# Performance work log

Hardware: AMD Instinct MI355X
Metric: run time of the kernel (lower is better)

The kernel has to match this reference:

```python
import jax, jax.numpy as jnp
import numpy as np

B, S, V, E, H, L = 64, 512, 32000, 512, 512, 2


def setup_inputs() -> dict:
    key = jax.random.key(0)
    ks = jax.random.split(key, 8)
    x = jax.random.randint(ks[0], (B, S), 0, V, dtype=jnp.int64 if jax.config.jax_enable_x64 else jnp.int32)
    # pack_right_padded_seq assumes right-padded seqs; hidden[:ebs] slicing implies
    # lengths sorted in DESCENDING order. Enforce length >= 1.
    lengths = jnp.clip(jax.random.randint(ks[1], (B,), 0, S + 1), 1, S)
    lengths = jnp.sort(lengths)[::-1]
    scale = 1.0 / np.sqrt(H)
    emb = jax.random.normal(ks[2], (V, E), dtype=jnp.float32) * 0.02
    W_ih = jax.random.uniform(ks[3], (L, H, E), jnp.float32, -scale, scale)
    W_hh = jax.random.uniform(ks[4], (L, H, H), jnp.float32, -scale, scale)
    b_ih = jax.random.uniform(ks[5], (L, H), jnp.float32, -scale, scale)
    b_hh = jax.random.uniform(ks[6], (L, H), jnp.float32, -scale, scale)
    return {"x": x, "lengths": lengths, "emb": emb, "W_ih": W_ih,
            "W_hh": W_hh, "b_ih": b_ih, "b_hh": b_hh}


def reference(x, lengths, emb, W_ih, W_hh, b_ih, b_hh):
    # Equivalent to the packed-sequence loop: at timestep t, only sequences with
    # t < length are active (packing with descending lengths keeps them as the
    # leading rows). We express the same math with a mask + lax.scan.
    xe = jnp.swapaxes(emb[x], 0, 1)                       # [S, B, E]
    mask = jnp.arange(S)[:, None] < lengths[None, :]      # [S, B]
    h0 = jnp.zeros((B, L, H), dtype=emb.dtype)

    def step(h, inp):
        xt, m = inp                                        # [B,E], [B]
        cur = xt
        hs = []
        for l in range(L):
            hl = h[:, l]                                   # [B, H]
            hn = jnp.tanh(cur @ W_ih[l].T + b_ih[l] + hl @ W_hh[l].T + b_hh[l])
            hl = jnp.where(m[:, None], hn, hl)             # freeze finished seqs
            hs.append(hl)
            cur = hl                                       # next layer's input
        return jnp.stack(hs, axis=1), None

    hidden, _ = jax.lax.scan(step, h0, (xe, mask))
    out = hidden[:, -1]                                    # last layer final state
    return out, hidden
```

## Files before the change

kernel.cpp:

```cpp
#include <hip/hip_runtime.h>


#define BATCH 64
#define SEQ   512
#define HID   512
#define NTHR  256
#define CB    8
#define ROWS  32
#define SLOT  (BATCH * HID)

typedef unsigned int u32;
typedef unsigned long long u64;
#define POISON 0xFFFFFFFFFFFFFFFFull

__device__ __forceinline__ float dot4(const float4 a, const float4 b) {
  return a.x * b.x + a.y * b.y + a.z * b.z + a.w * b.w;
}
__device__ __forceinline__ float2 ld2(const double* p) {
  const double d = __hip_atomic_load(p, __ATOMIC_RELAXED, __HIP_MEMORY_SCOPE_AGENT);
  return __builtin_bit_cast(float2, d);
}
__device__ __forceinline__ u64 ldu(const double* p) {
  const double d = __hip_atomic_load(p, __ATOMIC_RELAXED, __HIP_MEMORY_SCOPE_AGENT);
  return __builtin_bit_cast(u64, d);
}
__device__ __forceinline__ void st2(double* p, float2 v) {
  __hip_atomic_store(p, __builtin_bit_cast(double, v),
                     __ATOMIC_RELAXED, __HIP_MEMORY_SCOPE_AGENT);
}
__device__ __forceinline__ float tanh_fast(float x) {
  const float a = fabsf(x);
  const float e = __expf(-2.0f * a);
  const float t = (1.0f - e) * __builtin_amdgcn_rcpf(1.0f + e);
  return copysignf(t, x);
}
#define WAIT_VM0() asm volatile("s_waitcnt vmcnt(0)" ::: "memory")

#define RSTEP(D, N)                                                   \
  {                                                                   \
    const bool hi = (lane & (D)) != 0;                                \
    _Pragma("unroll")                                                 \
    for (int a = 0; a < (N); ++a) {                                   \
      const float keep = hi ? v[a + (N)] : v[a];                      \
      const float send = hi ? v[a] : v[a + (N)];                      \
      v[a] = keep + __shfl_xor(send, (D));                            \
    }                                                                 \
  }

template <bool NP>
__global__ __launch_bounds__(NTHR, 1) void rnn_persistent(
    const int* __restrict__ x, const int* __restrict__ lengths,
    const float* __restrict__ emb,
    const float* __restrict__ W_ih, const float* __restrict__ W_hh,
    const float* __restrict__ b_ih, const float* __restrict__ b_hh,
    float* __restrict__ out,
    float* h0r, float* h1r, u32* F, int ring)
{
  __shared__ __align__(16) float Xa[CB][HID];
  __shared__ __align__(16) float Xb[CB][HID];
  __shared__ __align__(16) float Xpart[CB][ROWS][4];
  __shared__ int Lens[CB];

  const int wg    = blockIdx.x;
  const int tid   = threadIdx.x;
  const int dom   = wg & 7;
  const int q     = wg >> 3;
  const int layer = q >> 4;
  const int rg    = q & 15;
  const int bbase = dom * CB;
  const int jbase = rg * ROWS;
  const int tj    = tid >> 6;
  const int lane  = tid & 63;

  u32* Fown = F + ((dom * 2 + layer) * 16 + rg) * 32;
  u32* F0   = F + ((dom * 2 + 0) * 16) * 32;
  u32* F1   = F + ((dom * 2 + 1) * 16) * 32;

  float4 wa[2][8], wb[2][8];
  {
    const float* WA = W_ih + layer * (HID * HID);
    const float* WB = W_hh + layer * (HID * HID);
    #pragma unroll
    for (int ji = 0; ji < 8; ++ji) {
      const int j = jbase + tj * 8 + ji;
      #pragma unroll
      for (int i = 0; i < 2; ++i) {
        const int k = i * 256 + 4 * lane;
        wa[i][ji] = *(const float4*)&WA[j * HID + k];
        wb[i][ji] = *(const float4*)&WB[j * HID + k];
      }
    }
  }
  if (tid < CB) Lens[tid] = lengths[bbase + tid];
  __syncthreads();
  int maxlen = Lens[0];
  #pragma unroll
  for (int i = 1; i < CB; ++i) maxlen = max(maxlen, Lens[i]);
  const int P     = maxlen;
  const int pl0   = (P < SEQ) ? P : (SEQ - 1);
  const int plast = layer ? P : pl0;
  int lm[4];
  #pragma unroll
  for (int g = 0; g < 4; ++g) lm[g] = max(Lens[2 * g], Lens[2 * g + 1]);

  float4 bias4 = make_float4(0.f, 0.f, 0.f, 0.f);
  if (tid < 64) {
    const int jq = jbase + (tid & 7) * 4;
    bias4.x = b_ih[layer * HID + jq + 0] + b_hh[layer * HID + jq + 0];
    bias4.y = b_ih[layer * HID + jq + 1] + b_hh[layer * HID + jq + 1];
    bias4.z = b_ih[layer * HID + jq + 2] + b_hh[layer * HID + jq + 2];
    bias4.w = b_ih[layer * HID + jq + 3] + b_hh[layer * HID + jq + 3];
  }

  float4 pf[4];
  if (layer == 0) {
    #pragma unroll
    for (int i = 0; i < 4; ++i) {
      const int u = tid + NTHR * i;
      const int r = u >> 7, c = (u & 127) * 4;
      const int tok = x[(bbase + r) * SEQ];
      pf[i] = *(const float4*)&emb[(size_t)tok * HID + c];
    }
  }

  int cur = 0, prev = ring - 1;

  for (int p = 0; p <= P; ++p) {
    const bool active = layer ? (p >= 1) : (p < SEQ);
    const int  wr0    = (cur + 1 == ring) ? 0 : (cur + 1);

    if (active) {
      const int t = layer ? (p - 1) : p;

      if (layer == 0) {
        const double* src = (const double*)(h0r) + (size_t)cur * (SLOT / 2);
        if constexpr (NP) {
          u64 tv[8];
          #pragma unroll
          for (int i = 0; i < 8; ++i) {
            const int u = tid + NTHR * i;
            tv[i] = ldu(&src[(size_t)(bbase + (u >> 8)) * 256 + (u & 255)]);
          }
          for (;;) {
            u32 bad = 0;
            #pragma unroll
            for (int i = 0; i < 8; ++i) bad |= (tv[i] == POISON) ? (1u << i) : 0u;
            if (!bad) break;
            #pragma unroll
            for (int i = 0; i < 8; ++i)
              if (bad & (1u << i)) {
                const int u = tid + NTHR * i;
                tv[i] = ldu(&src[(size_t)(bbase + (u >> 8)) * 256 + (u & 255)]);
              }
          }
          #pragma unroll
          for (int i = 0; i < 8; ++i) {
            const int u = tid + NTHR * i;
            *(float2*)&Xb[u >> 8][(u & 255) * 2] = __builtin_bit_cast(float2, tv[i]);
          }
        } else {
          float2 tv[8];
          #pragma unroll
          for (int i = 0; i < 8; ++i) {
            const int u = tid + NTHR * i;
            tv[i] = ld2(&src[(size_t)(bbase + (u >> 8)) * 256 + (u & 255)]);
          }
          #pragma unroll
          for (int i = 0; i < 8; ++i) {
            const int u = tid + NTHR * i;
            *(float2*)&Xb[u >> 8][(u & 255) * 2] = tv[i];
          }
        }
        #pragma unroll
        for (int i = 0; i < 4; ++i) {
          const int u = tid + NTHR * i;
          *(float4*)&Xa[u >> 7][(u & 127) * 4] = pf[i];
        }
      } else {
        const double* srcB = (const double*)(h1r) + (size_t)prev * (SLOT / 2);
        const double* srcA = (const double*)(h0r) + (size_t)cur  * (SLOT / 2);
        if constexpr (NP) {
          u64 tb[8], ta[8];
          #pragma unroll
          for (int i = 0; i < 8; ++i) {
            const int u = tid + NTHR * i;
            tb[i] = ldu(&srcB[(size_t)(bbase + (u >> 8)) * 256 + (u & 255)]);
          }
          #pragma unroll
          for (int i = 0; i < 8; ++i) {
            const int u = tid + NTHR * i;
            ta[i] = ldu(&srcA[(size_t)(bbase + (u >> 8)) * 256 + (u & 255)]);
          }
          for (;;) {
            u32 bad = 0;
            #pragma unroll
            for (int i = 0; i < 8; ++i) {
              bad |= (tb[i] == POISON) ? (1u << i) : 0u;
              bad |= (ta[i] == POISON) ? (1u << (i + 8)) : 0u;
            }
            if (!bad) break;
            #pragma unroll
            for (int i = 0; i < 8; ++i) {
              const int u = tid + NTHR * i;
              if (bad & (1u << i))
                tb[i] = ldu(&srcB[(size_t)(bbase + (u >> 8)) * 256 + (u & 255)]);
              if (bad & (1u << (i + 8)))
                ta[i] = ldu(&srcA[(size_t)(bbase + (u >> 8)) * 256 + (u & 255)]);
            }
          }
          #pragma unroll
          for (int i = 0; i < 8; ++i) {
            const int u = tid + NTHR * i;
            *(float2*)&Xb[u >> 8][(u & 255) * 2] = __builtin_bit_cast(float2, tb[i]);
            *(float2*)&Xa[u >> 8][(u & 255) * 2] = __builtin_bit_cast(float2, ta[i]);
          }
        } else {
          float2 tb[8], ta[8];
          #pragma unroll
          for (int i = 0; i < 8; ++i) {
            const int u = tid + NTHR * i;
            tb[i] = ld2(&srcB[(size_t)(bbase + (u >> 8)) * 256 + (u & 255)]);
          }
          #pragma unroll
          for (int i = 0; i < 8; ++i) {
            const int u = tid + NTHR * i;
            ta[i] = ld2(&srcA[(size_t)(bbase + (u >> 8)) * 256 + (u & 255)]);
          }
          #pragma unroll
          for (int i = 0; i < 8; ++i) {
            const int u = tid + NTHR * i;
            *(float2*)&Xb[u >> 8][(u & 255) * 2] = tb[i];
            *(float2*)&Xa[u >> 8][(u & 255) * 2] = ta[i];
          }
        }
      }
      __syncthreads();

      #pragma unroll 2
      for (int g = 0; g < 4; ++g) {
        if (t >= lm[g]) continue;
        float v[16];
        #pragma unroll
        for (int o = 0; o < 16; ++o) v[o] = 0.f;
        #pragma unroll
        for (int bi = 0; bi < 2; ++bi) {
          const int b = g * 2 + bi;
          const float4 xa0 = *(const float4*)&Xa[b][4 * lane];
          const float4 xa1 = *(const float4*)&Xa[b][256 + 4 * lane];
          const float4 xb0 = *(const float4*)&Xb[b][4 * lane];
          const float4 xb1 = *(const float4*)&Xb[b][256 + 4 * lane];
          #pragma unroll
          for (int ji = 0; ji < 8; ++ji) {
            v[bi * 8 + ji] += dot4(wa[0][ji], xa0) + dot4(wa[1][ji], xa1)
                            + dot4(wb[0][ji], xb0) + dot4(wb[1][ji], xb1);
          }
        }
        RSTEP(32, 8)
        RSTEP(16, 4)
        RSTEP(8, 2)
        RSTEP(4, 1)
        const int b_o = g * 2 + (lane >> 5);
        const int j_o = tj * 8 + ((lane >> 2) & 7);
        Xpart[b_o][j_o][lane & 3] = v[0];
      }
      __syncthreads();

      if (tid < 64) {
        const int b = tid >> 3, jq = (tid & 7) * 4;
        const float4 hb = *(const float4*)&Xb[b][jbase + jq];
        const bool live = (t < Lens[b]);
        float4 r = hb;
        if (live) {
          const float4 p0 = *(const float4*)&Xpart[b][jq + 0][0];
          const float4 p1 = *(const float4*)&Xpart[b][jq + 1][0];
          const float4 p2 = *(const float4*)&Xpart[b][jq + 2][0];
          const float4 p3 = *(const float4*)&Xpart[b][jq + 3][0];
          r.x = tanh_fast(p0.x + p0.y + p0.z + p0.w + bias4.x);
          r.y = tanh_fast(p1.x + p1.y + p1.z + p1.w + bias4.y);
          r.z = tanh_fast(p2.x + p2.y + p2.z + p2.w + bias4.z);
          r.w = tanh_fast(p3.x + p3.y + p3.z + p3.w + bias4.w);
        }
        double* dst = layer ? ((double*)h1r + (size_t)cur * (SLOT / 2))
                            : ((double*)h0r + (size_t)wr0 * (SLOT / 2));
        const size_t di = (size_t)(bbase + b) * 256 + ((jbase + jq) >> 1);
        st2(&dst[di],     make_float2(r.x, r.y));
        st2(&dst[di + 1], make_float2(r.z, r.w));
        if (p == plast) {
          if (layer == 0) {
            *(float4*)&out[32768 + (size_t)(bbase + b) * 1024 + jbase + jq] = r;
          } else {
            *(float4*)&out[(size_t)(bbase + b) * 512 + jbase + jq] = r;
            *(float4*)&out[32768 + (size_t)(bbase + b) * 1024 + 512 + jbase + jq] = r;
          }
        }
      }
    }

    if constexpr (NP) {
      const int np = p + 1;
      if (layer == 0 && np <= plast) {
        #pragma unroll
        for (int i = 0; i < 4; ++i) {
          const int u = tid + NTHR * i;
          const int r = u >> 7, c = (u & 127) * 4;
          const int tok = x[(bbase + r) * SEQ + np];
          pf[i] = *(const float4*)&emb[(size_t)tok * HID + c];
        }
      }
      __syncthreads();
    } else {
      WAIT_VM0();
      __syncthreads();
      if (tid == 0 && active)
        __hip_atomic_store(Fown, (u32)(layer ? p : (p + 1)),
                           __ATOMIC_RELAXED, __HIP_MEMORY_SCOPE_AGENT);
      const int np = p + 1;
      if (layer == 0 && np <= plast) {
        #pragma unroll
        for (int i = 0; i < 4; ++i) {
          const int u = tid + NTHR * i;
          const int r = u >> 7, c = (u & 127) * 4;
          const int tok = x[(bbase + r) * SEQ + np];
          pf[i] = *(const float4*)&emb[(size_t)tok * HID + c];
        }
      }
      if (np <= P) {
        if (tid < 64) {
          u32* fp  = Fown;
          u32  tgt = 0;
          bool idle = true;
          if (lane < 16) { fp = F0 + lane * 32; tgt = (u32)np; idle = false; }
          else if (lane < 32) {
            if (layer) { fp = F1 + (lane - 16) * 32; tgt = (u32)(np - 1); idle = false; }
            else {
              const int th = np + 1 - ring;
              if (th > 0) { fp = F1 + (lane - 16) * 32; tgt = (u32)th; idle = false; }
            }
          }
          while (true) {
            const u32 vv = __hip_atomic_load(fp, __ATOMIC_RELAXED,
                                             __HIP_MEMORY_SCOPE_AGENT);
            const bool ok = idle || (vv >= tgt);
            if (__ballot(ok) == ~0ull) break;
          }
        }
        __syncthreads();
      }
    }
    prev = cur; cur = wr0;
  }
}

extern "C" void kernel_launch(void* const* d_in, const int* in_sizes, int n_in,
                              void* d_out, int out_size, void* d_ws, size_t ws_size,
                              hipStream_t stream) {
  (void)in_sizes; (void)n_in; (void)out_size;
  const int*   x       = (const int*)d_in[0];
  const int*   lengths = (const int*)d_in[1];
  const float* emb     = (const float*)d_in[2];
  const float* W_ih    = (const float*)d_in[3];
  const float* W_hh    = (const float*)d_in[4];
  const float* b_ih    = (const float*)d_in[5];
  const float* b_hh    = (const float*)d_in[6];
  float* out = (float*)d_out;

  const size_t slotB = (size_t)SLOT * sizeof(float);
  const size_t needFull = 2 * (size_t)513 * slotB + 65536;
  const int ring = (ws_size >= needFull) ? 513 : 17;

  float* h0r = (float*)d_ws;
  float* h1r = h0r + (size_t)ring * SLOT;
  u32*   F   = (u32*)(h1r + (size_t)ring * SLOT);

  if (ring == 513) {
    hipMemsetAsync(h0r, 0xFF, 2 * (size_t)513 * slotB, stream);
    hipMemsetAsync(h0r, 0, slotB, stream);
    hipMemsetAsync(h1r, 0, slotB, stream);
    hipLaunchKernelGGL((rnn_persistent<true>), dim3(256), dim3(NTHR), 0, stream,
                       x, lengths, emb, W_ih, W_hh, b_ih, b_hh, out,
                       h0r, h1r, F, ring);
  } else {
    hipMemsetAsync(h0r, 0, slotB, stream);
    hipMemsetAsync(h1r, 0, slotB, stream);
    hipMemsetAsync(F, 0, 32768, stream);
    hipLaunchKernelGGL((rnn_persistent<false>), dim3(256), dim3(NTHR), 0, stream,
                       x, lengths, emb, W_ih, W_hh, b_ih, b_hh, out,
                       h0r, h1r, F, ring);
  }
}
```

Baseline: 3.240 ms.

## Replace poison-polling with flag sync using sc0 loads and an XCC-locality probe

```diff
diff --git a/kernel.cpp b/kernel.cpp
--- a/kernel.cpp
+++ b/kernel.cpp
@@ -11,14 +11,9 @@
 
 typedef unsigned int u32;
 typedef unsigned long long u64;
-#define POISON 0xFFFFFFFFFFFFFFFFull
 
 __device__ __forceinline__ float dot4(const float4 a, const float4 b) {
   return a.x * b.x + a.y * b.y + a.z * b.z + a.w * b.w;
-}
-__device__ __forceinline__ float2 ld2(const double* p) {
-  const double d = __hip_atomic_load(p, __ATOMIC_RELAXED, __HIP_MEMORY_SCOPE_AGENT);
-  return __builtin_bit_cast(float2, d);
 }
 __device__ __forceinline__ u64 ldu(const double* p) {
   const double d = __hip_atomic_load(p, __ATOMIC_RELAXED, __HIP_MEMORY_SCOPE_AGENT);
@@ -27,6 +22,23 @@
 __device__ __forceinline__ void st2(double* p, float2 v) {
   __hip_atomic_store(p, __builtin_bit_cast(double, v),
                      __ATOMIC_RELAXED, __HIP_MEMORY_SCOPE_AGENT);
+}
+__device__ __forceinline__ u64 ld8_sc0(const double* p) {
+  u64 r;
+  asm volatile("global_load_dwordx2 %0, %1, off sc0" : "=v"(r) : "v"(p) : "memory");
+  return r;
+}
+__device__ __forceinline__ void st8_sc0(double* p, u64 v) {
+  asm volatile("global_store_dwordx2 %0, %1, off sc0" :: "v"(p), "v"(v) : "memory");
+}
+__device__ __forceinline__ u32 ld_flag_sc0(const u32* p) {
+  u32 r;
+  asm volatile("global_load_dword %0, %1, off sc0\n\ts_waitcnt vmcnt(0)"
+               : "=v"(r) : "v"(p) : "memory");
+  return r;
+}
+__device__ __forceinline__ void st_flag_sc0(u32* p, u32 v) {
+  asm volatile("global_store_dword %0, %1, off sc0" :: "v"(p), "v"(v) : "memory");
 }
 __device__ __forceinline__ float tanh_fast(float x) {
   const float a = fabsf(x);
@@ -35,6 +47,7 @@
   return copysignf(t, x);
 }
 #define WAIT_VM0() asm volatile("s_waitcnt vmcnt(0)" ::: "memory")
+#define GETREG_XCC ((20) | (0 << 6) | (31 << 11))
 
 #define RSTEP(D, N)                                                   \
   {                                                                   \
@@ -47,7 +60,6 @@
     }                                                                 \
   }
 
-template <bool NP>
 __global__ __launch_bounds__(NTHR, 1) void rnn_persistent(
     const int* __restrict__ x, const int* __restrict__ lengths,
     const float* __restrict__ emb,
@@ -60,6 +72,7 @@
   __shared__ __align__(16) float Xb[CB][HID];
   __shared__ __align__(16) float Xpart[CB][ROWS][4];
   __shared__ int Lens[CB];
+  __shared__ int FastSh;
 
   const int wg    = blockIdx.x;
   const int tid   = threadIdx.x;
@@ -75,6 +88,17 @@
   u32* Fown = F + ((dom * 2 + layer) * 16 + rg) * 32;
   u32* F0   = F + ((dom * 2 + 0) * 16) * 32;
   u32* F1   = F + ((dom * 2 + 1) * 16) * 32;
+  u32* Tok = F + 8192 + dom * 32;
+  u32* Prf = F + 8448 + dom * 32;
+  u32* Vot = F + 8704 + dom * 32;
+  const int slot32 = layer * 16 + rg;
+
+  const int xcc = (int)(__builtin_amdgcn_s_getreg(GETREG_XCC) & 0xf);
+  if (tid == 0) {
+    __hip_atomic_store(&Tok[slot32], (u32)(xcc + 2),
+                       __ATOMIC_RELAXED, __HIP_MEMORY_SCOPE_AGENT);
+    st_flag_sc0(&Prf[slot32], 1u);
+  }
 
   float4 wa[2][8], wb[2][8];
   {
@@ -123,6 +147,48 @@
     }
   }
 
+  if (tid < 64) {
+    u32 tok = 0;
+    while (true) {
+      if (lane < 32 && tok == 0)
+        tok = __hip_atomic_load(&Tok[lane], __ATOMIC_RELAXED,
+                                __HIP_MEMORY_SCOPE_AGENT);
+      if (__ballot(lane >= 32 || tok != 0) == ~0ull) break;
+    }
+    const u32 t0 = __shfl(tok, 0);
+    const bool samex = (__ballot(lane >= 32 || tok == t0) == ~0ull);
+    bool ok = false;
+    if (samex) {
+      int budget = 6000;
+      bool fail = false;
+      for (int r = 1; r <= 4 && !fail; ++r) {
+        bool seen = (lane >= 32);
+        while (true) {
+          if (!seen) seen = (ld_flag_sc0(&Prf[lane]) >= (u32)r);
+          if (__ballot(seen) == ~0ull) break;
+          if (--budget <= 0) { fail = true; break; }
+        }
+        if (!fail && r < 4 && lane == 0)
+          st_flag_sc0(&Prf[slot32], (u32)(r + 1));
+      }
+      ok = !fail;
+    }
+    if (tid == 0)
+      __hip_atomic_store(&Vot[slot32], ok ? 2u : 1u,
+                         __ATOMIC_RELAXED, __HIP_MEMORY_SCOPE_AGENT);
+    u32 vv = 0;
+    while (true) {
+      if (lane < 32 && vv == 0)
+        vv = __hip_atomic_load(&Vot[lane], __ATOMIC_RELAXED,
+                               __HIP_MEMORY_SCOPE_AGENT);
+      if (__ballot(lane >= 32 || vv != 0) == ~0ull) break;
+    }
+    const bool allf = (__ballot(lane >= 32 || vv == 2) == ~0ull);
+    if (tid == 0) FastSh = allf ? 1 : 0;
+  }
+  __syncthreads();
+  const bool fast = (FastSh != 0);
+
   int cur = 0, prev = ring - 1;
 
   for (int p = 0; p <= P; ++p) {
@@ -134,42 +200,25 @@
 
       if (layer == 0) {
         const double* src = (const double*)(h0r) + (size_t)cur * (SLOT / 2);
-        if constexpr (NP) {
-          u64 tv[8];
+        u64 tv[8];
+        if (fast) {
+          #pragma unroll
+          for (int i = 0; i < 8; ++i) {
+            const int u = tid + NTHR * i;
+            tv[i] = ld8_sc0(&src[(size_t)(bbase + (u >> 8)) * 256 + (u & 255)]);
+          }
+          WAIT_VM0();
+        } else {
           #pragma unroll
           for (int i = 0; i < 8; ++i) {
             const int u = tid + NTHR * i;
             tv[i] = ldu(&src[(size_t)(bbase + (u >> 8)) * 256 + (u & 255)]);
           }
-          for (;;) {
-            u32 bad = 0;
-            #pragma unroll
-            for (int i = 0; i < 8; ++i) bad |= (tv[i] == POISON) ? (1u << i) : 0u;
-            if (!bad) break;
-            #pragma unroll
-            for (int i = 0; i < 8; ++i)
-              if (bad & (1u << i)) {
-                const int u = tid + NTHR * i;
-                tv[i] = ldu(&src[(size_t)(bbase + (u >> 8)) * 256 + (u & 255)]);
-              }
-          }
-          #pragma unroll
-          for (int i = 0; i < 8; ++i) {
-            const int u = tid + NTHR * i;
-            *(float2*)&Xb[u >> 8][(u & 255) * 2] = __builtin_bit_cast(float2, tv[i]);
-          }
-        } else {
-          float2 tv[8];
-          #pragma unroll
-          for (int i = 0; i < 8; ++i) {
-            const int u = tid + NTHR * i;
-            tv[i] = ld2(&src[(size_t)(bbase + (u >> 8)) * 256 + (u & 255)]);
-          }
-          #pragma unroll
-          for (int i = 0; i < 8; ++i) {
-            const int u = tid + NTHR * i;
-            *(float2*)&Xb[u >> 8][(u & 255) * 2] = tv[i];
-          }
+        }
+        #pragma unroll
+        for (int i = 0; i < 8; ++i) {
+          const int u = tid + NTHR * i;
+          *(float2*)&Xb[u >> 8][(u & 255) * 2] = __builtin_bit_cast(float2, tv[i]);
         }
         #pragma unroll
         for (int i = 0; i < 4; ++i) {
@@ -179,8 +228,20 @@
       } else {
         const double* srcB = (const double*)(h1r) + (size_t)prev * (SLOT / 2);
         const double* srcA = (const double*)(h0r) + (size_t)cur  * (SLOT / 2);
-        if constexpr (NP) {
-          u64 tb[8], ta[8];
+        u64 tb[8], ta[8];
+        if (fast) {
+          #pragma unroll
+          for (int i = 0; i < 8; ++i) {
+            const int u = tid + NTHR * i;
+            tb[i] = ld8_sc0(&srcB[(size_t)(bbase + (u >> 8)) * 256 + (u & 255)]);
+          }
+          #pragma unroll
+          for (int i = 0; i < 8; ++i) {
+            const int u = tid + NTHR * i;
+            ta[i] = ld8_sc0(&srcA[(size_t)(bbase + (u >> 8)) * 256 + (u & 255)]);
+          }
+          WAIT_VM0();
+        } else {
           #pragma unroll
           for (int i = 0; i < 8; ++i) {
             const int u = tid + NTHR * i;
@@ -191,47 +252,12 @@
             const int u = tid + NTHR * i;
             ta[i] = ldu(&srcA[(size_t)(bbase + (u >> 8)) * 256 + (u & 255)]);
           }
-          for (;;) {
-            u32 bad = 0;
-            #pragma unroll
-            for (int i = 0; i < 8; ++i) {
-              bad |= (tb[i] == POISON) ? (1u << i) : 0u;
-              bad |= (ta[i] == POISON) ? (1u << (i + 8)) : 0u;
-            }
-            if (!bad) break;
-            #pragma unroll
-            for (int i = 0; i < 8; ++i) {
-              const int u = tid + NTHR * i;
-              if (bad & (1u << i))
-                tb[i] = ldu(&srcB[(size_t)(bbase + (u >> 8)) * 256 + (u & 255)]);
-              if (bad & (1u << (i + 8)))
-                ta[i] = ldu(&srcA[(size_t)(bbase + (u >> 8)) * 256 + (u & 255)]);
-            }
-          }
-          #pragma unroll
-          for (int i = 0; i < 8; ++i) {
-            const int u = tid + NTHR * i;
-            *(float2*)&Xb[u >> 8][(u & 255) * 2] = __builtin_bit_cast(float2, tb[i]);
-            *(float2*)&Xa[u >> 8][(u & 255) * 2] = __builtin_bit_cast(float2, ta[i]);
-          }
-        } else {
-          float2 tb[8], ta[8];
-          #pragma unroll
-          for (int i = 0; i < 8; ++i) {
-            const int u = tid + NTHR * i;
-            tb[i] = ld2(&srcB[(size_t)(bbase + (u >> 8)) * 256 + (u & 255)]);
-          }
-          #pragma unroll
-          for (int i = 0; i < 8; ++i) {
-            const int u = tid + NTHR * i;
-            ta[i] = ld2(&srcA[(size_t)(bbase + (u >> 8)) * 256 + (u & 255)]);
-          }
-          #pragma unroll
-          for (int i = 0; i < 8; ++i) {
-            const int u = tid + NTHR * i;
-            *(float2*)&Xb[u >> 8][(u & 255) * 2] = tb[i];
-            *(float2*)&Xa[u >> 8][(u & 255) * 2] = ta[i];
-          }
+        }
+        #pragma unroll
+        for (int i = 0; i < 8; ++i) {
+          const int u = tid + NTHR * i;
+          *(float2*)&Xb[u >> 8][(u & 255) * 2] = __builtin_bit_cast(float2, tb[i]);
+          *(float2*)&Xa[u >> 8][(u & 255) * 2] = __builtin_bit_cast(float2, ta[i]);
         }
       }
       __syncthreads();
@@ -283,8 +309,13 @@
         double* dst = layer ? ((double*)h1r + (size_t)cur * (SLOT / 2))
                             : ((double*)h0r + (size_t)wr0 * (SLOT / 2));
         const size_t di = (size_t)(bbase + b) * 256 + ((jbase + jq) >> 1);
-        st2(&dst[di],     make_float2(r.x, r.y));
-        st2(&dst[di + 1], make_float2(r.z, r.w));
+        if (fast) {
+          st8_sc0(&dst[di],     __builtin_bit_cast(u64, make_float2(r.x, r.y)));
+          st8_sc0(&dst[di + 1], __builtin_bit_cast(u64, make_float2(r.z, r.w)));
+        } else {
+          st2(&dst[di],     make_float2(r.x, r.y));
+          st2(&dst[di + 1], make_float2(r.z, r.w));
+        }
         if (p == plast) {
           if (layer == 0) {
             *(float4*)&out[32768 + (size_t)(bbase + b) * 1024 + jbase + jq] = r;
@@ -296,56 +327,45 @@
       }
     }
 
-    if constexpr (NP) {
-      const int np = p + 1;
-      if (layer == 0 && np <= plast) {
-        #pragma unroll
-        for (int i = 0; i < 4; ++i) {
-          const int u = tid + NTHR * i;
-          const int r = u >> 7, c = (u & 127) * 4;
-          const int tok = x[(bbase + r) * SEQ + np];
-          pf[i] = *(const float4*)&emb[(size_t)tok * HID + c];
+    WAIT_VM0();
+    __syncthreads();
+    if (tid == 0 && active) {
+      const u32 fv = (u32)(layer ? p : (p + 1));
+      if (fast) st_flag_sc0(Fown, fv);
+      else __hip_atomic_store(Fown, fv, __ATOMIC_RELAXED, __HIP_MEMORY_SCOPE_AGENT);
+    }
+    const int np = p + 1;
+    if (layer == 0 && np <= plast) {
+      #pragma unroll
+      for (int i = 0; i < 4; ++i) {
+        const int u = tid + NTHR * i;
+        const int r = u >> 7, c = (u & 127) * 4;
+        const int tok = x[(bbase + r) * SEQ + np];
+        pf[i] = *(const float4*)&emb[(size_t)tok * HID + c];
+      }
+    }
+    if (np <= P) {
+      if (tid < 64) {
+        u32* fp  = Fown;
+        u32  tgt = 0;
+        bool idle = true;
+        if (lane < 16) { fp = F0 + lane * 32; tgt = (u32)np; idle = false; }
+        else if (lane < 32) {
+          if (layer) { fp = F1 + (lane - 16) * 32; tgt = (u32)(np - 1); idle = false; }
+          else {
+            const int th = np + 1 - ring;
+            if (th > 0) { fp = F1 + (lane - 16) * 32; tgt = (u32)th; idle = false; }
+          }
+        }
+        while (true) {
+          const u32 vv = fast ? ld_flag_sc0(fp)
+                              : __hip_atomic_load(fp, __ATOMIC_RELAXED,
+                                                  __HIP_MEMORY_SCOPE_AGENT);
+          const bool ok = idle || (vv >= tgt);
+          if (__ballot(ok) == ~0ull) break;
         }
       }
       __syncthreads();
-    } else {
-      WAIT_VM0();
-      __syncthreads();
-      if (tid == 0 && active)
-        __hip_atomic_store(Fown, (u32)(layer ? p : (p + 1)),
-                           __ATOMIC_RELAXED, __HIP_MEMORY_SCOPE_AGENT);
-      const int np = p + 1;
-      if (layer == 0 && np <= plast) {
-        #pragma unroll
-        for (int i = 0; i < 4; ++i) {
-          const int u = tid + NTHR * i;
-          const int r = u >> 7, c = (u & 127) * 4;
-          const int tok = x[(bbase + r) * SEQ + np];
-          pf[i] = *(const float4*)&emb[(size_t)tok * HID + c];
-        }
-      }
-      if (np <= P) {
-        if (tid < 64) {
-          u32* fp  = Fown;
-          u32  tgt = 0;
-          bool idle = true;
-          if (lane < 16) { fp = F0 + lane * 32; tgt = (u32)np; idle = false; }
-          else if (lane < 32) {
-            if (layer) { fp = F1 + (lane - 16) * 32; tgt = (u32)(np - 1); idle = false; }
-            else {
-              const int th = np + 1 - ring;
-              if (th > 0) { fp = F1 + (lane - 16) * 32; tgt = (u32)th; idle = false; }
-            }
-          }
-          while (true) {
-            const u32 vv = __hip_atomic_load(fp, __ATOMIC_RELAXED,
-                                             __HIP_MEMORY_SCOPE_AGENT);
-            const bool ok = idle || (vv >= tgt);
-            if (__ballot(ok) == ~0ull) break;
-          }
-        }
-        __syncthreads();
-      }
     }
     prev = cur; cur = wr0;
   }
@@ -364,27 +384,19 @@
   const float* b_hh    = (const float*)d_in[6];
   float* out = (float*)d_out;
 
-  const size_t slotB = (size_t)SLOT * sizeof(float);
-  const size_t needFull = 2 * (size_t)513 * slotB + 65536;
-  const int ring = (ws_size >= needFull) ? 513 : 17;
+  const size_t slotB  = (size_t)SLOT * sizeof(float);
+  const size_t need64 = 2 * (size_t)64 * slotB + 65536;
+  const int ring = (ws_size >= need64) ? 64 : 17;
 
   float* h0r = (float*)d_ws;
   float* h1r = h0r + (size_t)ring * SLOT;
   u32*   F   = (u32*)(h1r + (size_t)ring * SLOT);
 
-  if (ring == 513) {
-    hipMemsetAsync(h0r, 0xFF, 2 * (size_t)513 * slotB, stream);
-    hipMemsetAsync(h0r, 0, slotB, stream);
-    hipMemsetAsync(h1r, 0, slotB, stream);
-    hipLaunchKernelGGL((rnn_persistent<true>), dim3(256), dim3(NTHR), 0, stream,
-                       x, lengths, emb, W_ih, W_hh, b_ih, b_hh, out,
-                       h0r, h1r, F, ring);
-  } else {
-    hipMemsetAsync(h0r, 0, slotB, stream);
-    hipMemsetAsync(h1r, 0, slotB, stream);
-    hipMemsetAsync(F, 0, 32768, stream);
-    hipLaunchKernelGGL((rnn_persistent<false>), dim3(256), dim3(NTHR), 0, stream,
-                       x, lengths, emb, W_ih, W_hh, b_ih, b_hh, out,
-                       h0r, h1r, F, ring);
-  }
-}
+  hipMemsetAsync(h0r, 0, slotB, stream);
+  hipMemsetAsync(h1r, 0, slotB, stream);
+  hipMemsetAsync(F, 0, 65536, stream);
+
+  hipLaunchKernelGGL(rnn_persistent, dim3(256), dim3(NTHR), 0, stream,
+                     x, lengths, emb, W_ih, W_hh, b_ih, b_hh, out,
+                     h0r, h1r, F, ring);
+}
```

New measurement: 3.763 ms. +16.1%, slower.

## Replace poison-value polling with flag-based synchronization and sleep in spin loop

Applied to the files above, without the earlier changes.

```diff
diff --git a/kernel.cpp b/kernel.cpp
--- a/kernel.cpp
+++ b/kernel.cpp
@@ -10,8 +10,6 @@
 #define SLOT  (BATCH * HID)
 
 typedef unsigned int u32;
-typedef unsigned long long u64;
-#define POISON 0xFFFFFFFFFFFFFFFFull
 
 __device__ __forceinline__ float dot4(const float4 a, const float4 b) {
   return a.x * b.x + a.y * b.y + a.z * b.z + a.w * b.w;
@@ -19,10 +17,6 @@
 __device__ __forceinline__ float2 ld2(const double* p) {
   const double d = __hip_atomic_load(p, __ATOMIC_RELAXED, __HIP_MEMORY_SCOPE_AGENT);
   return __builtin_bit_cast(float2, d);
-}
-__device__ __forceinline__ u64 ldu(const double* p) {
-  const double d = __hip_atomic_load(p, __ATOMIC_RELAXED, __HIP_MEMORY_SCOPE_AGENT);
-  return __builtin_bit_cast(u64, d);
 }
 __device__ __forceinline__ void st2(double* p, float2 v) {
   __hip_atomic_store(p, __builtin_bit_cast(double, v),
@@ -47,7 +41,6 @@
     }                                                                 \
   }
 
-template <bool NP>
 __global__ __launch_bounds__(NTHR, 1) void rnn_persistent(
     const int* __restrict__ x, const int* __restrict__ lengths,
     const float* __restrict__ emb,
@@ -134,42 +127,16 @@
 
       if (layer == 0) {
         const double* src = (const double*)(h0r) + (size_t)cur * (SLOT / 2);
-        if constexpr (NP) {
-          u64 tv[8];
-          #pragma unroll
-          for (int i = 0; i < 8; ++i) {
-            const int u = tid + NTHR * i;
-            tv[i] = ldu(&src[(size_t)(bbase + (u >> 8)) * 256 + (u & 255)]);
-          }
-          for (;;) {
-            u32 bad = 0;
-            #pragma unroll
-            for (int i = 0; i < 8; ++i) bad |= (tv[i] == POISON) ? (1u << i) : 0u;
-            if (!bad) break;
-            #pragma unroll
-            for (int i = 0; i < 8; ++i)
-              if (bad & (1u << i)) {
-                const int u = tid + NTHR * i;
-                tv[i] = ldu(&src[(size_t)(bbase + (u >> 8)) * 256 + (u & 255)]);
-              }
-          }
-          #pragma unroll
-          for (int i = 0; i < 8; ++i) {
-            const int u = tid + NTHR * i;
-            *(float2*)&Xb[u >> 8][(u & 255) * 2] = __builtin_bit_cast(float2, tv[i]);
-          }
-        } else {
-          float2 tv[8];
-          #pragma unroll
-          for (int i = 0; i < 8; ++i) {
-            const int u = tid + NTHR * i;
-            tv[i] = ld2(&src[(size_t)(bbase + (u >> 8)) * 256 + (u & 255)]);
-          }
-          #pragma unroll
-          for (int i = 0; i < 8; ++i) {
-            const int u = tid + NTHR * i;
-            *(float2*)&Xb[u >> 8][(u & 255) * 2] = tv[i];
-          }
+        float2 tv[8];
+        #pragma unroll
+        for (int i = 0; i < 8; ++i) {
+          const int u = tid + NTHR * i;
+          tv[i] = ld2(&src[(size_t)(bbase + (u >> 8)) * 256 + (u & 255)]);
+        }
+        #pragma unroll
+        for (int i = 0; i < 8; ++i) {
+          const int u = tid + NTHR * i;
+          *(float2*)&Xb[u >> 8][(u & 255) * 2] = tv[i];
         }
         #pragma unroll
         for (int i = 0; i < 4; ++i) {
@@ -179,59 +146,22 @@
       } else {
         const double* srcB = (const double*)(h1r) + (size_t)prev * (SLOT / 2);
         const double* srcA = (const double*)(h0r) + (size_t)cur  * (SLOT / 2);
-        if constexpr (NP) {
-          u64 tb[8], ta[8];
-          #pragma unroll
-          for (int i = 0; i < 8; ++i) {
-            const int u = tid + NTHR * i;
-            tb[i] = ldu(&srcB[(size_t)(bbase + (u >> 8)) * 256 + (u & 255)]);
-          }
-          #pragma unroll
-          for (int i = 0; i < 8; ++i) {
-            const int u = tid + NTHR * i;
-            ta[i] = ldu(&srcA[(size_t)(bbase + (u >> 8)) * 256 + (u & 255)]);
-          }
-          for (;;) {
-            u32 bad = 0;
-            #pragma unroll
-            for (int i = 0; i < 8; ++i) {
-              bad |= (tb[i] == POISON) ? (1u << i) : 0u;
-              bad |= (ta[i] == POISON) ? (1u << (i + 8)) : 0u;
-            }
-            if (!bad) break;
-            #pragma unroll
-            for (int i = 0; i < 8; ++i) {
-              const int u = tid + NTHR * i;
-              if (bad & (1u << i))
-                tb[i] = ldu(&srcB[(size_t)(bbase + (u >> 8)) * 256 + (u & 255)]);
-              if (bad & (1u << (i + 8)))
-                ta[i] = ldu(&srcA[(size_t)(bbase + (u >> 8)) * 256 + (u & 255)]);
-            }
-          }
-          #pragma unroll
-          for (int i = 0; i < 8; ++i) {
-            const int u = tid + NTHR * i;
-            *(float2*)&Xb[u >> 8][(u & 255) * 2] = __builtin_bit_cast(float2, tb[i]);
-            *(float2*)&Xa[u >> 8][(u & 255) * 2] = __builtin_bit_cast(float2, ta[i]);
-          }
-        } else {
-          float2 tb[8], ta[8];
-          #pragma unroll
-          for (int i = 0; i < 8; ++i) {
-            const int u = tid + NTHR * i;
-            tb[i] = ld2(&srcB[(size_t)(bbase + (u >> 8)) * 256 + (u & 255)]);
-          }
-          #pragma unroll
-          for (int i = 0; i < 8; ++i) {
-            const int u = tid + NTHR * i;
-            ta[i] = ld2(&srcA[(size_t)(bbase + (u >> 8)) * 256 + (u & 255)]);
-          }
-          #pragma unroll
-          for (int i = 0; i < 8; ++i) {
-            const int u = tid + NTHR * i;
-            *(float2*)&Xb[u >> 8][(u & 255) * 2] = tb[i];
-            *(float2*)&Xa[u >> 8][(u & 255) * 2] = ta[i];
-          }
+        float2 tb[8], ta[8];
+        #pragma unroll
+        for (int i = 0; i < 8; ++i) {
+          const int u = tid + NTHR * i;
+          tb[i] = ld2(&srcB[(size_t)(bbase + (u >> 8)) * 256 + (u & 255)]);
+        }
+        #pragma unroll
+        for (int i = 0; i < 8; ++i) {
+          const int u = tid + NTHR * i;
+          ta[i] = ld2(&srcA[(size_t)(bbase + (u >> 8)) * 256 + (u & 255)]);
+        }
+        #pragma unroll
+        for (int i = 0; i < 8; ++i) {
+          const int u = tid + NTHR * i;
+          *(float2*)&Xb[u >> 8][(u & 255) * 2] = tb[i];
+          *(float2*)&Xa[u >> 8][(u & 255) * 2] = ta[i];
         }
       }
       __syncthreads();
@@ -296,56 +226,42 @@
       }
     }
 
-    if constexpr (NP) {
-      const int np = p + 1;
-      if (layer == 0 && np <= plast) {
-        #pragma unroll
-        for (int i = 0; i < 4; ++i) {
-          const int u = tid + NTHR * i;
-          const int r = u >> 7, c = (u & 127) * 4;
-          const int tok = x[(bbase + r) * SEQ + np];
-          pf[i] = *(const float4*)&emb[(size_t)tok * HID + c];
+    WAIT_VM0();
+    if (tid == 0 && active)
+      __hip_atomic_store(Fown, (u32)(layer ? p : (p + 1)),
+                         __ATOMIC_RELAXED, __HIP_MEMORY_SCOPE_AGENT);
+    __syncthreads();
+    const int np = p + 1;
+    if (layer == 0 && np <= plast) {
+      #pragma unroll
+      for (int i = 0; i < 4; ++i) {
+        const int u = tid + NTHR * i;
+        const int r = u >> 7, c = (u & 127) * 4;
+        const int tok = x[(bbase + r) * SEQ + np];
+        pf[i] = *(const float4*)&emb[(size_t)tok * HID + c];
+      }
+    }
+    if (np <= P) {
+      if (tid < 64) {
+        u32* fp  = Fown;
+        u32  tgt = 0;
+        bool ok  = true;
+        if (lane < 16) { fp = F0 + lane * 32; tgt = (u32)np; ok = false; }
+        else if (lane < 32) {
+          if (layer) { fp = F1 + (lane - 16) * 32; tgt = (u32)(np - 1); ok = false; }
+          else {
+            const int th = np + 1 - ring;
+            if (th > 0) { fp = F1 + (lane - 16) * 32; tgt = (u32)th; ok = false; }
+          }
+        }
+        while (true) {
+          if (!ok) ok = (__hip_atomic_load(fp, __ATOMIC_RELAXED,
+                                           __HIP_MEMORY_SCOPE_AGENT) >= tgt);
+          if (__ballot(ok) == ~0ull) break;
+          __builtin_amdgcn_s_sleep(1);
         }
       }
       __syncthreads();
-    } else {
-      WAIT_VM0();
-      __syncthreads();
-      if (tid == 0 && active)
-        __hip_atomic_store(Fown, (u32)(layer ? p : (p + 1)),
-                           __ATOMIC_RELAXED, __HIP_MEMORY_SCOPE_AGENT);
-      const int np = p + 1;
-      if (layer == 0 && np <= plast) {
-        #pragma unroll
-        for (int i = 0; i < 4; ++i) {
-          const int u = tid + NTHR * i;
-          const int r = u >> 7, c = (u & 127) * 4;
-          const int tok = x[(bbase + r) * SEQ + np];
-          pf[i] = *(const float4*)&emb[(size_t)tok * HID + c];
-        }
-      }
-      if (np <= P) {
-        if (tid < 64) {
-          u32* fp  = Fown;
-          u32  tgt = 0;
-          bool idle = true;
-          if (lane < 16) { fp = F0 + lane * 32; tgt = (u32)np; idle = false; }
-          else if (lane < 32) {
-            if (layer) { fp = F1 + (lane - 16) * 32; tgt = (u32)(np - 1); idle = false; }
-            else {
-              const int th = np + 1 - ring;
-              if (th > 0) { fp = F1 + (lane - 16) * 32; tgt = (u32)th; idle = false; }
-            }
-          }
-          while (true) {
-            const u32 vv = __hip_atomic_load(fp, __ATOMIC_RELAXED,
-                                             __HIP_MEMORY_SCOPE_AGENT);
-            const bool ok = idle || (vv >= tgt);
-            if (__ballot(ok) == ~0ull) break;
-          }
-        }
-        __syncthreads();
-      }
     }
     prev = cur; cur = wr0;
   }
@@ -372,19 +288,11 @@
   float* h1r = h0r + (size_t)ring * SLOT;
   u32*   F   = (u32*)(h1r + (size_t)ring * SLOT);
 
-  if (ring == 513) {
-    hipMemsetAsync(h0r, 0xFF, 2 * (size_t)513 * slotB, stream);
-    hipMemsetAsync(h0r, 0, slotB, stream);
-    hipMemsetAsync(h1r, 0, slotB, stream);
-    hipLaunchKernelGGL((rnn_persistent<true>), dim3(256), dim3(NTHR), 0, stream,
-                       x, lengths, emb, W_ih, W_hh, b_ih, b_hh, out,
-                       h0r, h1r, F, ring);
-  } else {
-    hipMemsetAsync(h0r, 0, slotB, stream);
-    hipMemsetAsync(h1r, 0, slotB, stream);
-    hipMemsetAsync(F, 0, 32768, stream);
-    hipLaunchKernelGGL((rnn_persistent<false>), dim3(256), dim3(NTHR), 0, stream,
-                       x, lengths, emb, W_ih, W_hh, b_ih, b_hh, out,
-                       h0r, h1r, F, ring);
-  }
-}
+  hipMemsetAsync(h0r, 0, slotB, stream);
+  hipMemsetAsync(h1r, 0, slotB, stream);
+  hipMemsetAsync(F, 0, 32768, stream);
+
+  hipLaunchKernelGGL(rnn_persistent, dim3(256), dim3(NTHR), 0, stream,
+                     x, lengths, emb, W_ih, W_hh, b_ih, b_hh, out,
+                     h0r, h1r, F, ring);
+}
```

Result: faster. 2.919 ms (-9.9%).
